# Optimization experiments

Hardware: AMD Instinct MI355X
Metric: run time of the kernel (lower is better)

Reference implementation:

```python
import jax, jax.numpy as jnp
import numpy as np

DIM, HEADS, HD, FFN = 1536, 12, 128, 8960
B, F, H, W = 1, 4, 20, 32
S = F * H * W          # 2560 latent tokens
L2 = 512               # text context length
EPS = 1e-6


def _ln(x):
    m = jnp.mean(x, -1, keepdims=True)
    v = jnp.mean(jnp.square(x - m), -1, keepdims=True)
    return (x - m) * jax.lax.rsqrt(v + EPS)


def _rms(x, g):
    return x * jax.lax.rsqrt(jnp.mean(jnp.square(x), -1, keepdims=True) + EPS) * g


def _dyn_quant(x):
    # per-token symmetric int8 dynamic activation quantization (A8, dynamic input scale)
    s = jnp.maximum(jnp.max(jnp.abs(x), -1, keepdims=True) / 127.0, 1e-8)
    q = jnp.clip(jnp.round(x / s), -127.0, 127.0)
    return q, s, jnp.sum(q, -1)   # sum_input used for asymmetric-weight zero-point correction


def _quant_w(w):
    # per-output-channel asymmetric int8 weight quantization (weight_sym=False)
    wmin = jnp.min(w, 1, keepdims=True)
    wmax = jnp.max(w, 1, keepdims=True)
    s = jnp.maximum((wmax - wmin) / 255.0, 1e-8)
    zp = jnp.round(-128.0 - wmin / s)
    qw = jnp.clip(jnp.round(w / s) + zp, -128.0, 127.0)
    return qw, s[:, 0], zp[:, 0]


def _w8a8(qx, s_x, sum_qx, w, b):
    # y = s_x * s_w * (qx @ (qw - zp)^T) + b = s_x*s_w*(qx@qw^T - zp*sum(qx)) + b
    qw, sw, zp = _quant_w(w)
    acc = jnp.einsum('bsi,oi->bso', qx, qw) - sum_qx[..., None] * zp
    return acc * s_x * sw + b


def _rope(x, fr, f, h, w):
    # x: [B,S,N,D] with S == f*h*w; fr: [1024, D//2] complex rope table
    Bn, Sn, N, D = x.shape
    c = D // 2
    s0 = c - 2 * (c // 3)
    fF = jnp.broadcast_to(fr[:f, :s0].reshape(f, 1, 1, s0), (f, h, w, s0))
    fH = jnp.broadcast_to(fr[:h, s0:s0 + c // 3].reshape(1, h, 1, c // 3), (f, h, w, c // 3))
    fW = jnp.broadcast_to(fr[:w, s0 + c // 3:].reshape(1, 1, w, c // 3), (f, h, w, c // 3))
    fi = jnp.concatenate([fF, fH, fW], -1).reshape(1, f * h * w, 1, c)
    xr = x.reshape(Bn, Sn, N, c, 2)
    xc = jax.lax.complex(xr[..., 0], xr[..., 1]) * fi
    return jnp.stack([jnp.real(xc), jnp.imag(xc)], -1).reshape(Bn, Sn, N, D)


def _attn(q, k, v, k_lens):
    scale = 1.0 / jnp.sqrt(jnp.float32(q.shape[-1]))
    scores = jnp.einsum('bqnd,bknd->bnqk', q, k) * scale
    mask = jnp.arange(k.shape[1])[None, None, None, :] < k_lens[:, None, None, None]
    p = jax.nn.softmax(jnp.where(mask, scores, -1e30), -1)
    return jnp.einsum('bnqk,bknd->bqnd', p, v)


def _forward(x, e, freqs, context, modulation,
             wq, bq, wk, bk, wv, bv, wo, bo, gq, gk, n3_w, n3_b,
             cwq, cbq, cwk, cbk, cwv, cbv, cwo, cbo, cgq, cgk,
             w1, b1, w2, b2, f, h, w, seq_lens, context_lens):
    fr = jax.lax.complex(freqs[..., 0], freqs[..., 1])
    em = modulation + e  # [B,6,C]
    sm, sc, gm, smlp, scmlp, gmlp = [em[:, i:i + 1] for i in range(6)]
    Bn, Sn, C = x.shape
    # --- self attention: fused norm+modulation then shared per-token int8 quant for q/k/v ---
    h1 = _ln(x) * (1.0 + sc) + sm
    qx, s_x, sum_qx = _dyn_quant(h1)
    q = _rms(_w8a8(qx, s_x, sum_qx, wq, bq), gq).reshape(Bn, Sn, HEADS, HD)
    k = _rms(_w8a8(qx, s_x, sum_qx, wk, bk), gk).reshape(Bn, Sn, HEADS, HD)
    v = _w8a8(qx, s_x, sum_qx, wv, bv).reshape(Bn, Sn, HEADS, HD)
    q = _rope(q, fr, f, h, w)
    k = _rope(k, fr, f, h, w)
    y = _attn(q, k, v, seq_lens).reshape(Bn, Sn, C) @ wo.T + bo
    x = x + y * gm
    # --- cross attention (fp16/fp path in the original; use_kernel[1]=False) ---
    hx = _ln(x) * n3_w + n3_b
    cq = _rms(hx @ cwq.T + cbq, cgq).reshape(Bn, Sn, HEADS, HD)
    ck = _rms(context @ cwk.T + cbk, cgk).reshape(Bn, L2, HEADS, HD)
    cv = (context @ cwv.T + cbv).reshape(Bn, L2, HEADS, HD)
    y = _attn(cq, ck, cv, context_lens).reshape(Bn, Sn, C) @ cwo.T + cbo
    x = x + y
    # --- FFN with modulation (use_kernel[2]=False) ---
    h2 = _ln(x) * (1.0 + scmlp) + smlp
    y = jax.nn.gelu(h2 @ w1.T + b1, approximate=True) @ w2.T + b2
    return x + y * gmlp


def setup_inputs():
    key = jax.random.key(0)
    ks = jax.random.split(key, 16)

    def P(i, shape, s=0.02):
        return jax.random.normal(ks[i], shape, jnp.float32) * s

    x = jax.random.normal(ks[0], (B, S, DIM), jnp.float32)
    e = jax.random.normal(ks[1], (B, 6, DIM), jnp.float32)
    context = jax.random.normal(ks[2], (B, L2, DIM), jnp.float32)
    seq_lens = jnp.array([S], jnp.int32)
    grid_sizes = jnp.array([[F, H, W]], jnp.int32)
    context_lens = jnp.array([L2], jnp.int32)
    c = HD // 2
    pos = np.arange(1024, dtype=np.float64)[:, None]
    theta = 1.0 / (10000.0 ** (np.arange(c, dtype=np.float64) / c))
    ang = pos * theta
    freqs = jnp.asarray(np.stack([np.cos(ang), np.sin(ang)], -1), jnp.float32)
    z = lambda n: jnp.zeros((n,), jnp.float32)
    o = lambda n: jnp.ones((n,), jnp.float32)
    return dict(x=x, e=e, seq_lens=seq_lens, grid_sizes=grid_sizes, freqs=freqs,
                context=context, context_lens=context_lens,
                modulation=P(3, (1, 6, DIM), 1.0 / DIM ** 0.5),
                wq=P(4, (DIM, DIM)), bq=z(DIM), wk=P(5, (DIM, DIM)), bk=z(DIM),
                wv=P(6, (DIM, DIM)), bv=z(DIM), wo=P(7, (DIM, DIM)), bo=z(DIM),
                gq=o(DIM), gk=o(DIM), n3_w=o(DIM), n3_b=z(DIM),
                cwq=P(8, (DIM, DIM)), cbq=z(DIM), cwk=P(9, (DIM, DIM)), cbk=z(DIM),
                cwv=P(10, (DIM, DIM)), cbv=z(DIM), cwo=P(11, (DIM, DIM)), cbo=z(DIM),
                cgq=o(DIM), cgk=o(DIM),
                w1=P(12, (FFN, DIM)), b1=z(FFN), w2=P(13, (DIM, FFN)), b2=z(DIM))


def reference(x, e, seq_lens, grid_sizes, freqs, context, context_lens, modulation,
              wq, bq, wk, bk, wv, bv, wo, bo, gq, gk, n3_w, n3_b,
              cwq, cbq, cwk, cbk, cwv, cbv, cwo, cbo, cgq, cgk,
              w1, b1, w2, b2):
    f, h, w = int(grid_sizes[0, 0]), int(grid_sizes[0, 1]), int(grid_sizes[0, 2])
    return _forward(x, e, freqs, context, modulation,
                    wq, bq, wk, bk, wv, bv, wo, bo, gq, gk, n3_w, n3_b,
                    cwq, cbq, cwk, cbk, cwv, cbv, cwo, cbo, cgq, cgk,
                    w1, b1, w2, b2, f, h, w, seq_lens, context_lens)
```

## Files before the change

### kernel.cpp

```cpp
#include <hip/hip_runtime.h>
#include <stdint.h>


typedef unsigned short u16;
typedef __bf16 bf16x8 __attribute__((ext_vector_type(8)));
typedef float f32x4 __attribute__((ext_vector_type(4)));

#define DEV __device__ __forceinline__

DEV u16 f2b(float f) {
  uint32_t u = __float_as_uint(f);
  u += 0x7fffu + ((u >> 16) & 1u);
  return (u16)(u >> 16);
}

DEV float gelu_tanh(float v) {
  float u = 0.7978845608028654f * (v + 0.044715f * v * v * v);
  return 0.5f * v * (1.0f + tanhf(u));
}

DEV void gl_lds16(const u16* g, u16* l) {
  __builtin_amdgcn_global_load_lds(
      (const __attribute__((address_space(1))) void*)g,
      (__attribute__((address_space(3))) void*)l, 16, 0, 0);
}

DEV float bred_sum(float v, float* scr) {
  #pragma unroll
  for (int o = 32; o; o >>= 1) v += __shfl_down(v, o, 64);
  if ((threadIdx.x & 63) == 0) scr[threadIdx.x >> 6] = v;
  __syncthreads();
  v = scr[0] + scr[1] + scr[2] + scr[3];
  __syncthreads();
  return v;
}
DEV float bred_max(float v, float* scr) {
  #pragma unroll
  for (int o = 32; o; o >>= 1) v = fmaxf(v, __shfl_down(v, o, 64));
  if ((threadIdx.x & 63) == 0) scr[threadIdx.x >> 6] = v;
  __syncthreads();
  v = fmaxf(fmaxf(scr[0], scr[1]), fmaxf(scr[2], scr[3]));
  __syncthreads();
  return v;
}
DEV float bred_min(float v, float* scr) {
  #pragma unroll
  for (int o = 32; o; o >>= 1) v = fminf(v, __shfl_down(v, o, 64));
  if ((threadIdx.x & 63) == 0) scr[threadIdx.x >> 6] = v;
  __syncthreads();
  v = fminf(fminf(scr[0], scr[1]), fminf(scr[2], scr[3]));
  __syncthreads();
  return v;
}

__global__ __launch_bounds__(256) void pack_kernel(
    const float* __restrict__ e, const float* __restrict__ mod,
    const float* __restrict__ cbk, const float* __restrict__ cbv,
    float* __restrict__ em, float* __restrict__ bckv) {
  int i = blockIdx.x * 256 + threadIdx.x;
  if (i < 9216) em[i] = e[i] + mod[i];
  if (i < 3072) bckv[i] = (i < 1536) ? cbk[i] : cbv[i - 1536];
}

__global__ __launch_bounds__(256) void cvt_bf16_kernel(
    const float* __restrict__ in, u16* __restrict__ out, int n4) {
  int stride = gridDim.x * 256;
  for (int i = blockIdx.x * 256 + threadIdx.x; i < n4; i += stride) {
    float4 v = ((const float4*)in)[i];
    uint2 r;
    r.x = (uint32_t)f2b(v.x) | ((uint32_t)f2b(v.y) << 16);
    r.y = (uint32_t)f2b(v.z) | ((uint32_t)f2b(v.w) << 16);
    ((uint2*)out)[i] = r;
  }
}

__global__ __launch_bounds__(256) void ln_quant_kernel(
    const float* __restrict__ x, const float* __restrict__ em,
    u16* __restrict__ qx, float* __restrict__ sx, float* __restrict__ sumq) {
  __shared__ float scr[4];
  const int row = blockIdx.x, tid = threadIdx.x;
  const float* xr = x + (size_t)row * 1536;
  float v[6], s = 0.f, s2 = 0.f;
  #pragma unroll
  for (int t = 0; t < 6; t++) { v[t] = xr[tid + t * 256]; s += v[t]; s2 += v[t] * v[t]; }
  s = bred_sum(s, scr); s2 = bred_sum(s2, scr);
  float mean = s / 1536.f;
  float var = s2 / 1536.f - mean * mean;
  float inv = rsqrtf(var + 1e-6f);
  float hv[6], amax = 0.f;
  #pragma unroll
  for (int t = 0; t < 6; t++) {
    int i = tid + t * 256;
    hv[t] = (v[t] - mean) * inv * (1.f + em[1536 + i]) + em[i];
    amax = fmaxf(amax, fabsf(hv[t]));
  }
  amax = bred_max(amax, scr);
  float sxv = fmaxf(amax / 127.f, 1e-8f);
  float qs = 0.f;
  #pragma unroll
  for (int t = 0; t < 6; t++) {
    int i = tid + t * 256;
    float q = fminf(fmaxf(rintf(hv[t] / sxv), -127.f), 127.f);
    qs += q;
    qx[(size_t)row * 1536 + i] = f2b(q);
  }
  qs = bred_sum(qs, scr);
  if (tid == 0) { sx[row] = sxv; sumq[row] = qs; }
}

__global__ __launch_bounds__(256) void quantw_kernel(
    const float* __restrict__ wq, const float* __restrict__ wk, const float* __restrict__ wv,
    const float* __restrict__ bq, const float* __restrict__ bk, const float* __restrict__ bv,
    u16* __restrict__ qw, float* __restrict__ sw, float* __restrict__ zp, float* __restrict__ ball) {
  __shared__ float scr[4];
  const int row = blockIdx.x, tid = threadIdx.x;
  const int sel = (row >= 3072) ? 2 : (row >= 1536 ? 1 : 0);
  const int r = row - sel * 1536;
  const float* w = sel == 0 ? wq : (sel == 1 ? wk : wv);
  const float* bb = sel == 0 ? bq : (sel == 1 ? bk : bv);
  const float* wr = w + (size_t)r * 1536;
  float v[6], mn = 1e30f, mx = -1e30f;
  #pragma unroll
  for (int t = 0; t < 6; t++) { v[t] = wr[tid + t * 256]; mn = fminf(mn, v[t]); mx = fmaxf(mx, v[t]); }
  mn = bred_min(mn, scr); mx = bred_max(mx, scr);
  float s = fmaxf((mx - mn) / 255.f, 1e-8f);
  float z = rintf(-128.f - mn / s);
  #pragma unroll
  for (int t = 0; t < 6; t++) {
    int i = tid + t * 256;
    float q = fminf(fmaxf(rintf(v[t] / s) + z, -128.f), 127.f);
    qw[(size_t)row * 1536 + i] = f2b(q);
  }
  if (tid == 0) { sw[row] = s; zp[row] = z; ball[row] = bb[r]; }
}

template<int EP>
DEV void gemm_epilogue(float v, int row, int col, int N, void* Cout,
                       const float* bias, const float* sxp, const float* sumqp,
                       const float* swp, const float* zpp,
                       const float* gp, const float* residp) {
  size_t idx = (size_t)row * N + col;
  if constexpr (EP == 0) {
    ((float*)Cout)[idx] = v + bias[col];
  } else if constexpr (EP == 1) {
    v = (v - sumqp[row] * zpp[col]) * (sxp[row] * swp[col]) + bias[col];
    ((float*)Cout)[idx] = v;
  } else if constexpr (EP == 2) {
    v += bias[col];
    if (gp) v *= gp[col];
    ((float*)Cout)[idx] = v + residp[idx];
  } else if constexpr (EP == 3) {
    ((u16*)Cout)[idx] = f2b(gelu_tanh(v + bias[col]));
  } else {
    ((float*)Cout)[idx] = v;
  }
}

template<int EP>
__global__ __launch_bounds__(256) void gemm_bt_kernel(
    const u16* __restrict__ A, const u16* __restrict__ B, void* __restrict__ Cout,
    int N, int K, const float* __restrict__ bias,
    const float* __restrict__ sxp, const float* __restrict__ sumqp,
    const float* __restrict__ swp, const float* __restrict__ zpp,
    const float* __restrict__ gp, const float* __restrict__ residp) {
  __shared__ __align__(16) u16 As[128 * 32];
  __shared__ __align__(16) u16 Bs[128 * 32];
  const int tid = threadIdx.x;
  const int wave = tid >> 6, lane = tid & 63;
  const int wm = wave >> 1, wn = wave & 1;
  const int quad = lane >> 4, l16 = lane & 15;
  const int m0 = blockIdx.y * 128, n0 = blockIdx.x * 128;

  int srow[2], scol[2];
  #pragma unroll
  for (int i = 0; i < 2; i++) {
    int row = (wave * 2 + i) * 16 + (lane >> 2);
    int chunk = ((lane & 3) - (row >> 1)) & 3;
    srow[i] = row; scol[i] = chunk * 8;
  }

  f32x4 acc[4][4];
  #pragma unroll
  for (int i = 0; i < 4; i++)
    #pragma unroll
    for (int j = 0; j < 4; j++) acc[i][j] = (f32x4){0.f, 0.f, 0.f, 0.f};

  for (int k0 = 0; k0 < K; k0 += 32) {
    #pragma unroll
    for (int i = 0; i < 2; i++) {
      gl_lds16(A + (size_t)(m0 + srow[i]) * K + k0 + scol[i], &As[(wave * 2 + i) * 512]);
      gl_lds16(B + (size_t)(n0 + srow[i]) * K + k0 + scol[i], &Bs[(wave * 2 + i) * 512]);
    }
    __syncthreads();
    bf16x8 af[4], bfv[4];
    #pragma unroll
    for (int mi = 0; mi < 4; mi++) {
      int row = wm * 64 + mi * 16 + l16;
      af[mi] = *(const bf16x8*)&As[row * 32 + (((quad + (row >> 1)) & 3) * 8)];
    }
    #pragma unroll
    for (int ni = 0; ni < 4; ni++) {
      int row = wn * 64 + ni * 16 + l16;
      bfv[ni] = *(const bf16x8*)&Bs[row * 32 + (((quad + (row >> 1)) & 3) * 8)];
    }
    #pragma unroll
    for (int mi = 0; mi < 4; mi++)
      #pragma unroll
      for (int ni = 0; ni < 4; ni++)
        acc[mi][ni] = __builtin_amdgcn_mfma_f32_16x16x32_bf16(af[mi], bfv[ni], acc[mi][ni], 0, 0, 0);
    __syncthreads();
  }
  #pragma unroll
  for (int mi = 0; mi < 4; mi++)
    #pragma unroll
    for (int ni = 0; ni < 4; ni++) {
      int col = n0 + wn * 64 + ni * 16 + l16;
      #pragma unroll
      for (int r = 0; r < 4; r++)
        gemm_epilogue<EP>(acc[mi][ni][r], m0 + wm * 64 + mi * 16 + quad * 4 + r, col,
                          N, Cout, bias, sxp, sumqp, swp, zpp, gp, residp);
    }
}

template<int EP>
__global__ __launch_bounds__(256) void gemm64_bt_kernel(
    const u16* __restrict__ A, const u16* __restrict__ B,
    void* __restrict__ Cout, void* __restrict__ Cout2, int N, int K, int KC,
    const float* __restrict__ bias,
    const float* __restrict__ sxp, const float* __restrict__ sumqp,
    const float* __restrict__ swp, const float* __restrict__ zpp,
    const float* __restrict__ gp, const float* __restrict__ residp) {
  __shared__ __align__(16) u16 As[2][64 * 64];
  __shared__ __align__(16) u16 Bs[2][128 * 64];
  const int tid = threadIdx.x;
  const int wave = tid >> 6, lane = tid & 63;
  const int wm = wave >> 1, wn = wave & 1;
  const int quad = lane >> 4, l16 = lane & 15;
  const int m0 = blockIdx.y * 64, n0 = blockIdx.x * 128;
  const int kstart = blockIdx.z * KC;

  int arow[2], acol[2], brow[4], bcol[4];
  #pragma unroll
  for (int i = 0; i < 2; i++) {
    int row = (wave * 2 + i) * 8 + (lane >> 3);
    arow[i] = row; acol[i] = (((lane & 7) - (row >> 1)) & 7) * 8;
  }
  #pragma unroll
  for (int i = 0; i < 4; i++) {
    int row = (wave * 4 + i) * 8 + (lane >> 3);
    brow[i] = row; bcol[i] = (((lane & 7) - (row >> 1)) & 7) * 8;
  }

  f32x4 acc[2][4];
  #pragma unroll
  for (int i = 0; i < 2; i++)
    #pragma unroll
    for (int j = 0; j < 4; j++) acc[i][j] = (f32x4){0.f, 0.f, 0.f, 0.f};

  const int nk = KC >> 6;
  auto stage = [&](int buf, int k0) {
    #pragma unroll
    for (int i = 0; i < 2; i++)
      gl_lds16(A + (size_t)(m0 + arow[i]) * K + kstart + k0 + acol[i],
               &As[buf][(wave * 2 + i) * 512]);
    #pragma unroll
    for (int i = 0; i < 4; i++)
      gl_lds16(B + (size_t)(n0 + brow[i]) * K + kstart + k0 + bcol[i],
               &Bs[buf][(wave * 4 + i) * 512]);
  };
  stage(0, 0);
  for (int kt = 0; kt < nk; kt++) {
    __syncthreads();
    const int cur = kt & 1;
    if (kt + 1 < nk) stage(1 - cur, (kt + 1) << 6);
    #pragma unroll
    for (int s = 0; s < 2; s++) {
      bf16x8 af[2], bfv[4];
      #pragma unroll
      for (int mi = 0; mi < 2; mi++) {
        int row = wm * 32 + mi * 16 + l16;
        int slot = ((s * 4 + quad) + (row >> 1)) & 7;
        af[mi] = *(const bf16x8*)&As[cur][row * 64 + slot * 8];
      }
      #pragma unroll
      for (int ni = 0; ni < 4; ni++) {
        int row = wn * 64 + ni * 16 + l16;
        int slot = ((s * 4 + quad) + (row >> 1)) & 7;
        bfv[ni] = *(const bf16x8*)&Bs[cur][row * 64 + slot * 8];
      }
      #pragma unroll
      for (int mi = 0; mi < 2; mi++)
        #pragma unroll
        for (int ni = 0; ni < 4; ni++)
          acc[mi][ni] = __builtin_amdgcn_mfma_f32_16x16x32_bf16(af[mi], bfv[ni], acc[mi][ni], 0, 0, 0);
    }
  }
  void* Cuse = (EP == 4 && blockIdx.z) ? Cout2 : Cout;
  #pragma unroll
  for (int mi = 0; mi < 2; mi++)
    #pragma unroll
    for (int ni = 0; ni < 4; ni++) {
      int col = n0 + wn * 64 + ni * 16 + l16;
      #pragma unroll
      for (int r = 0; r < 4; r++)
        gemm_epilogue<EP>(acc[mi][ni][r], m0 + wm * 32 + mi * 16 + quad * 4 + r, col,
                          N, Cuse, bias, sxp, sumqp, swp, zpp, gp, residp);
    }
}

__global__ __launch_bounds__(256) void splitk_reduce_kernel(
    const float* __restrict__ P0, const float* __restrict__ P1,
    float* __restrict__ out, const float* __restrict__ bias,
    const float* __restrict__ g, const float* __restrict__ resid,
    int N, int n4) {
  int stride = gridDim.x * 256;
  for (int i = blockIdx.x * 256 + threadIdx.x; i < n4; i += stride) {
    float4 a = ((const float4*)P0)[i];
    float4 b = ((const float4*)P1)[i];
    float4 r = ((const float4*)resid)[i];
    int col = (i * 4) % N;
    float4 o;
    o.x = (a.x + b.x + bias[col]) * g[col] + r.x;
    o.y = (a.y + b.y + bias[col + 1]) * g[col + 1] + r.y;
    o.z = (a.z + b.z + bias[col + 2]) * g[col + 2] + r.z;
    o.w = (a.w + b.w + bias[col + 3]) * g[col + 3] + r.w;
    ((float4*)out)[i] = o;
  }
}

__global__ __launch_bounds__(256) void rmsrope_b_kernel(
    const float* __restrict__ qkv, u16* __restrict__ qkvb,
    const float* __restrict__ gq, const float* __restrict__ gk,
    const float* __restrict__ freqs, const int* __restrict__ gsz) {
  __shared__ float scr[4];
  const int row = blockIdx.x, tid = threadIdx.x;
  const float* base = qkv + (size_t)row * 4608;
  u16* ob = qkvb + (size_t)row * 4608;
  const int gh = gsz[1], gw = gsz[2];
  const int hw = gh * gw;
  const int fi = row / hw, rem = row - fi * hw;
  const int hi = rem / gw, wi = rem - hi * gw;
  #pragma unroll
  for (int part = 0; part < 2; part++) {
    const float* p = base + part * 1536;
    u16* o = ob + part * 1536;
    const float* g = part ? gk : gq;
    const float sc = part ? 1.f : 0.08838834764831845f;
    float v[6], s2 = 0.f;
    #pragma unroll
    for (int t = 0; t < 6; t++) { v[t] = p[tid + t * 256]; s2 += v[t] * v[t]; }
    s2 = bred_sum(s2, scr);
    float inv = rsqrtf(s2 / 1536.f + 1e-6f);
    #pragma unroll
    for (int t = 0; t < 3; t++) {
      int pr = tid + t * 256;
      int c = pr & 63;
      int frow = (c < 22) ? fi : (c < 43 ? hi : wi);
      const float* fr = freqs + ((size_t)frow * 64 + c) * 2;
      float cv = fr[0], sv = fr[1];
      float x0 = p[2 * pr] * inv * g[2 * pr];
      float x1 = p[2 * pr + 1] * inv * g[2 * pr + 1];
      o[2 * pr] = f2b((x0 * cv - x1 * sv) * sc);
      o[2 * pr + 1] = f2b((x0 * sv + x1 * cv) * sc);
    }
  }
  #pragma unroll
  for (int t = 0; t < 6; t++) {
    int i = tid + t * 256;
    ob[3072 + i] = f2b(base[3072 + i]);
  }
}

__global__ __launch_bounds__(256) void rms_bf16_kernel(
    const float* __restrict__ X, u16* __restrict__ O, const float* __restrict__ g,
    int ldi, int ldo, float scale) {
  __shared__ float scr[4];
  const int row = blockIdx.x, tid = threadIdx.x;
  const float* xr = X + (size_t)row * ldi;
  u16* orow = O + (size_t)row * ldo;
  float v[6], s2 = 0.f;
  #pragma unroll
  for (int t = 0; t < 6; t++) { v[t] = xr[tid + t * 256]; s2 += v[t] * v[t]; }
  s2 = bred_sum(s2, scr);
  float inv = rsqrtf(s2 / 1536.f + 1e-6f) * scale;
  #pragma unroll
  for (int t = 0; t < 6; t++) {
    int i = tid + t * 256;
    orow[i] = f2b(v[t] * inv * g[i]);
  }
}

__global__ __launch_bounds__(256) void vtrans_kernel(
    const float* __restrict__ V, int ld, u16* __restrict__ Vt, int Skv) {
  __shared__ u16 T[64 * 136];
  const int h = blockIdx.y, k0 = blockIdx.x * 64, tid = threadIdx.x;
  #pragma unroll
  for (int i = 0; i < 8; i++) {
    int f4 = i * 256 + tid;
    int row = f4 >> 5, c4 = f4 & 31;
    float4 v = *(const float4*)(V + (size_t)(k0 + row) * ld + h * 128 + c4 * 4);
    ushort4 b;
    b.x = f2b(v.x); b.y = f2b(v.y); b.z = f2b(v.z); b.w = f2b(v.w);
    *(ushort4*)&T[row * 136 + c4 * 4] = b;
  }
  __syncthreads();
  #pragma unroll
  for (int i = 0; i < 4; i++) {
    int f8 = i * 256 + tid;
    int hd = f8 >> 3, kc = f8 & 7;
    u16 tmp[8];
    #pragma unroll
    for (int j = 0; j < 8; j++) tmp[j] = T[(kc * 8 + j) * 136 + hd];
    *(uint4*)(Vt + ((size_t)h * 128 + hd) * Skv + k0 + kc * 8) = *(const uint4*)tmp;
  }
}

__global__ __launch_bounds__(256) void fattn_kernel(
    const u16* __restrict__ Q, int ldq, const u16* __restrict__ Kg, int ldk,
    const u16* __restrict__ Vtg, u16* __restrict__ O, int ldo,
    const int* __restrict__ klen_ptr, int kmax) {
  __shared__ __align__(16) u16 Qs[64 * 136];
  __shared__ __align__(16) u16 Ks[64 * 136];
  __shared__ __align__(16) u16 Vt[128 * 72];
  __shared__ __align__(16) u16 Pt[4][16 * 72];
  const int tid = threadIdx.x, wave = tid >> 6, lane = tid & 63;
  const int quad = lane >> 4, l16 = lane & 15;
  const int h = blockIdx.y;
  const int q0 = blockIdx.x * 64;
  int klen = klen_ptr[0]; if (klen > kmax) klen = kmax;
  const u16* vbase = Vtg + (size_t)h * 128 * kmax;

  #pragma unroll
  for (int i = 0; i < 4; i++) {
    int c8 = i * 256 + tid;
    int row = c8 >> 4, cc = (c8 & 15) * 8;
    *(uint4*)&Qs[row * 136 + cc] = *(const uint4*)(Q + (size_t)(q0 + row) * ldq + h * 128 + cc);
  }
  __syncthreads();
  bf16x8 qf[4];
  #pragma unroll
  for (int s = 0; s < 4; s++)
    qf[s] = *(const bf16x8*)&Qs[(wave * 16 + l16) * 136 + s * 32 + quad * 8];

  float m_r[4] = {-1e30f, -1e30f, -1e30f, -1e30f};
  float l_r[4] = {0.f, 0.f, 0.f, 0.f};
  f32x4 oacc[8];
  #pragma unroll
  for (int n8 = 0; n8 < 8; n8++) oacc[n8] = (f32x4){0.f, 0.f, 0.f, 0.f};

  const int ktiles = (klen + 63) >> 6;
  for (int kt = 0; kt < ktiles; kt++) {
    const int k0 = kt * 64;
    __syncthreads();
    #pragma unroll
    for (int i = 0; i < 4; i++) {
      int c8 = i * 256 + tid;
      int row = c8 >> 4, cc = (c8 & 15) * 8;
      *(uint4*)&Ks[row * 136 + cc] = *(const uint4*)(Kg + (size_t)(k0 + row) * ldk + h * 128 + cc);
    }
    #pragma unroll
    for (int i = 0; i < 4; i++) {
      int f8 = i * 256 + tid;
      int hd = f8 >> 3, kc = f8 & 7;
      *(uint4*)&Vt[hd * 72 + kc * 8] = *(const uint4*)(vbase + (size_t)hd * kmax + k0 + kc * 8);
    }
    __syncthreads();
    f32x4 sacc[4];
    #pragma unroll
    for (int ni = 0; ni < 4; ni++) sacc[ni] = (f32x4){0.f, 0.f, 0.f, 0.f};
    #pragma unroll
    for (int ni = 0; ni < 4; ni++)
      #pragma unroll
      for (int s = 0; s < 4; s++) {
        bf16x8 kf = *(const bf16x8*)&Ks[(ni * 16 + l16) * 136 + s * 32 + quad * 8];
        sacc[ni] = __builtin_amdgcn_mfma_f32_16x16x32_bf16(qf[s], kf, sacc[ni], 0, 0, 0);
      }
    float alpha_r[4];
    #pragma unroll
    for (int r = 0; r < 4; r++) {
      float mx = -1e30f;
      #pragma unroll
      for (int ni = 0; ni < 4; ni++) {
        int col = k0 + ni * 16 + l16;
        float sv = (col < klen) ? sacc[ni][r] : -1e30f;
        sacc[ni][r] = sv;
        mx = fmaxf(mx, sv);
      }
      #pragma unroll
      for (int off = 1; off < 16; off <<= 1) mx = fmaxf(mx, __shfl_xor(mx, off, 64));
      float mnew = fmaxf(m_r[r], mx);
      float alpha = __expf(m_r[r] - mnew);
      float rsum = 0.f;
      float pv[4];
      #pragma unroll
      for (int ni = 0; ni < 4; ni++) {
        float p = __expf(sacc[ni][r] - mnew);
        pv[ni] = p;
        rsum += p;
      }
      #pragma unroll
      for (int off = 1; off < 16; off <<= 1) rsum += __shfl_xor(rsum, off, 64);
      l_r[r] = l_r[r] * alpha + rsum;
      m_r[r] = mnew;
      alpha_r[r] = alpha;
      #pragma unroll
      for (int ni = 0; ni < 4; ni++)
        Pt[wave][(quad * 4 + r) * 72 + ni * 16 + l16] = f2b(pv[ni]);
    }
    #pragma unroll
    for (int n8 = 0; n8 < 8; n8++)
      #pragma unroll
      for (int r = 0; r < 4; r++) oacc[n8][r] *= alpha_r[r];
    #pragma unroll
    for (int s2 = 0; s2 < 2; s2++) {
      bf16x8 pf = *(const bf16x8*)&Pt[wave][l16 * 72 + s2 * 32 + quad * 8];
      #pragma unroll
      for (int n8 = 0; n8 < 8; n8++) {
        bf16x8 vf = *(const bf16x8*)&Vt[(n8 * 16 + l16) * 72 + s2 * 32 + quad * 8];
        oacc[n8] = __builtin_amdgcn_mfma_f32_16x16x32_bf16(pf, vf, oacc[n8], 0, 0, 0);
      }
    }
  }
  float rl[4];
  #pragma unroll
  for (int r = 0; r < 4; r++) rl[r] = 1.f / l_r[r];
  #pragma unroll
  for (int n8 = 0; n8 < 8; n8++)
    #pragma unroll
    for (int r = 0; r < 4; r++) {
      int row = q0 + wave * 16 + quad * 4 + r;
      O[(size_t)row * ldo + h * 128 + n8 * 16 + l16] = f2b(oacc[n8][r] * rl[r]);
    }
}

__global__ __launch_bounds__(256) void ln_affine_kernel(
    const float* __restrict__ X, u16* __restrict__ O,
    const float* __restrict__ w, const float* __restrict__ b, float addone) {
  __shared__ float scr[4];
  const int row = blockIdx.x, tid = threadIdx.x;
  const float* xr = X + (size_t)row * 1536;
  float v[6], s = 0.f, s2 = 0.f;
  #pragma unroll
  for (int t = 0; t < 6; t++) { v[t] = xr[tid + t * 256]; s += v[t]; s2 += v[t] * v[t]; }
  s = bred_sum(s, scr); s2 = bred_sum(s2, scr);
  float mean = s / 1536.f;
  float inv = rsqrtf(s2 / 1536.f - mean * mean + 1e-6f);
  #pragma unroll
  for (int t = 0; t < 6; t++) {
    int i = tid + t * 256;
    O[(size_t)row * 1536 + i] = f2b((v[t] - mean) * inv * (addone + w[i]) + b[i]);
  }
}

extern "C" void kernel_launch(void* const* d_in, const int* in_sizes, int n_in,
                              void* d_out, int out_size, void* d_ws, size_t ws_size,
                              hipStream_t stream) {
  (void)in_sizes; (void)n_in; (void)out_size; (void)ws_size;
  const int S = 2560, D = 1536, L2C = 512, FF = 8960, ND = 4608, CKV = 3072;

  const float* x = (const float*)d_in[0];
  const float* e = (const float*)d_in[1];
  const int* seq_lens = (const int*)d_in[2];
  const int* grid_sz = (const int*)d_in[3];
  const float* freqs = (const float*)d_in[4];
  const float* context = (const float*)d_in[5];
  const int* ctx_lens = (const int*)d_in[6];
  const float* modulation = (const float*)d_in[7];
  const float* wq = (const float*)d_in[8];  const float* bq = (const float*)d_in[9];
  const float* wk = (const float*)d_in[10]; const float* bk = (const float*)d_in[11];
  const float* wv = (const float*)d_in[12]; const float* bv = (const float*)d_in[13];
  const float* wo = (const float*)d_in[14]; const float* bo = (const float*)d_in[15];
  const float* gq = (const float*)d_in[16]; const float* gk = (const float*)d_in[17];
  const float* n3w = (const float*)d_in[18]; const float* n3b = (const float*)d_in[19];
  const float* cwq = (const float*)d_in[20]; const float* cbq = (const float*)d_in[21];
  const float* cwk = (const float*)d_in[22]; const float* cbk = (const float*)d_in[23];
  const float* cwv = (const float*)d_in[24]; const float* cbv = (const float*)d_in[25];
  const float* cwo = (const float*)d_in[26]; const float* cbo = (const float*)d_in[27];
  const float* cgq = (const float*)d_in[28]; const float* cgk = (const float*)d_in[29];
  const float* w1 = (const float*)d_in[30]; const float* b1 = (const float*)d_in[31];
  const float* w2 = (const float*)d_in[32]; const float* b2 = (const float*)d_in[33];

  char* wsb = (char*)d_ws;
  size_t off = 0;
  auto alloc = [&](size_t bytes) -> void* {
    void* r = wsb + off;
    off += (bytes + 255) & ~(size_t)255;
    return r;
  };
  float* em   = (float*)alloc((size_t)6 * D * 4);
  float* bckv = (float*)alloc((size_t)CKV * 4);
  float* ball = (float*)alloc((size_t)ND * 4);
  float* sx   = (float*)alloc((size_t)S * 4);
  float* sumq = (float*)alloc((size_t)S * 4);
  float* sw   = (float*)alloc((size_t)ND * 4);
  float* zp   = (float*)alloc((size_t)ND * 4);
  u16* qx     = (u16*)alloc((size_t)S * D * 2);
  u16* qw     = (u16*)alloc((size_t)ND * D * 2);
  float* qkv  = (float*)alloc((size_t)S * ND * 4);
  u16* qkvb   = (u16*)alloc((size_t)S * ND * 2);
  u16* attnb  = (u16*)alloc((size_t)S * D * 2);
  u16* hx     = (u16*)alloc((size_t)S * D * 2);
  float* cq   = (float*)alloc((size_t)S * D * 4);
  float* ckv  = (float*)alloc((size_t)L2C * CKV * 4);
  u16* ctxb   = (u16*)alloc((size_t)L2C * D * 2);
  u16* cattn  = (u16*)alloc((size_t)S * D * 2);
  u16* wo_b   = (u16*)alloc((size_t)D * D * 2);
  u16* cwq_b  = (u16*)alloc((size_t)D * D * 2);
  u16* cwkv_b = (u16*)alloc((size_t)2 * D * D * 2);
  u16* cwo_b  = (u16*)alloc((size_t)D * D * 2);
  u16* w1_b   = (u16*)alloc((size_t)FF * D * 2);
  u16* w2_b   = (u16*)alloc((size_t)D * FF * 2);
  u16* h3 = (u16*)qkv;
  u16* h2 = attnb;
  u16* vtg = qw;
  u16* cvtg = qx;
  u16* cqb = hx;
  u16* ckvb = ctxb;
  float* x2 = cq;
  float* x1 = (float*)d_out;
  float* outp = (float*)d_out;
  float* P0 = (float*)qx;
  float* P1 = (float*)qkvb;

  auto cvt = [&](const float* in, u16* op, size_t n) {
    int n4 = (int)(n / 4);
    int blocks = (n4 + 255) / 256; if (blocks > 4096) blocks = 4096;
    cvt_bf16_kernel<<<blocks, 256, 0, stream>>>(in, op, n4);
  };

  pack_kernel<<<36, 256, 0, stream>>>(e, modulation, cbk, cbv, em, bckv);
  cvt(wo, wo_b, (size_t)D * D);
  cvt(cwq, cwq_b, (size_t)D * D);
  cvt(cwk, cwkv_b, (size_t)D * D);
  cvt(cwv, cwkv_b + (size_t)D * D, (size_t)D * D);
  cvt(cwo, cwo_b, (size_t)D * D);
  cvt(w1, w1_b, (size_t)FF * D);
  cvt(w2, w2_b, (size_t)D * FF);
  cvt(context, ctxb, (size_t)L2C * D);

  ln_quant_kernel<<<S, 256, 0, stream>>>(x, em, qx, sx, sumq);
  quantw_kernel<<<ND, 256, 0, stream>>>(wq, wk, wv, bq, bk, bv, qw, sw, zp, ball);

  gemm_bt_kernel<1><<<dim3(ND / 128, S / 128), 256, 0, stream>>>(
      qx, qw, qkv, ND, D, ball, sx, sumq, sw, zp, nullptr, nullptr);

  rmsrope_b_kernel<<<S, 256, 0, stream>>>(qkv, qkvb, gq, gk, freqs, grid_sz);
  vtrans_kernel<<<dim3(S / 64, 12), 256, 0, stream>>>(qkv + 3072, ND, vtg, S);

  fattn_kernel<<<dim3(S / 64, 12), 256, 0, stream>>>(
      qkvb, ND, qkvb + 1536, ND, vtg, attnb, D, seq_lens, S);

  gemm64_bt_kernel<2><<<dim3(D / 128, S / 64), 256, 0, stream>>>(
      attnb, wo_b, x1, nullptr, D, D, D, bo, nullptr, nullptr, nullptr, nullptr, em + 2 * D, x);

  ln_affine_kernel<<<S, 256, 0, stream>>>(x1, hx, n3w, n3b, 0.f);

  gemm64_bt_kernel<0><<<dim3(D / 128, S / 64), 256, 0, stream>>>(
      hx, cwq_b, cq, nullptr, D, D, D, cbq, nullptr, nullptr, nullptr, nullptr, nullptr, nullptr);
  gemm64_bt_kernel<0><<<dim3(CKV / 128, L2C / 64), 256, 0, stream>>>(
      ctxb, cwkv_b, ckv, nullptr, CKV, D, D, bckv, nullptr, nullptr, nullptr, nullptr, nullptr, nullptr);

  rms_bf16_kernel<<<S, 256, 0, stream>>>(cq, cqb, cgq, D, D, 0.08838834764831845f);
  rms_bf16_kernel<<<L2C, 256, 0, stream>>>(ckv, ckvb, cgk, CKV, D, 1.f);
  vtrans_kernel<<<dim3(L2C / 64, 12), 256, 0, stream>>>(ckv + 1536, CKV, cvtg, L2C);

  fattn_kernel<<<dim3(S / 64, 12), 256, 0, stream>>>(
      cqb, D, ckvb, D, cvtg, cattn, D, ctx_lens, L2C);

  gemm64_bt_kernel<2><<<dim3(D / 128, S / 64), 256, 0, stream>>>(
      cattn, cwo_b, x2, nullptr, D, D, D, cbo, nullptr, nullptr, nullptr, nullptr, nullptr, x1);

  ln_affine_kernel<<<S, 256, 0, stream>>>(x2, h2, em + 4 * D, em + 3 * D, 1.f);

  gemm_bt_kernel<3><<<dim3(FF / 128, S / 128), 256, 0, stream>>>(
      h2, w1_b, h3, FF, D, b1, nullptr, nullptr, nullptr, nullptr, nullptr, nullptr);

  gemm64_bt_kernel<4><<<dim3(D / 128, S / 64, 2), 256, 0, stream>>>(
      h3, w2_b, P0, P1, D, FF, FF / 2, nullptr, nullptr, nullptr, nullptr, nullptr, nullptr, nullptr);
  splitk_reduce_kernel<<<960, 256, 0, stream>>>(
      P0, P1, outp, b2, em + 5 * D, x2, D, S * D / 4);
}
```

Baseline: 941.5 us.

## Replace 128-tile GEMMs with 256x256 double-buffered 8-wave GEMM, split-K by four

```diff
diff --git a/kernel.cpp b/kernel.cpp
--- a/kernel.cpp
+++ b/kernel.cpp
@@ -156,69 +156,137 @@
   }
 }
 
+struct PtrQuad { void* p0; void* p1; void* p2; void* p3; };
+
 template<int EP>
-__global__ __launch_bounds__(256) void gemm_bt_kernel(
-    const u16* __restrict__ A, const u16* __restrict__ B, void* __restrict__ Cout,
-    int N, int K, const float* __restrict__ bias,
+__global__ __launch_bounds__(512, 2) void gemm256_bt_kernel(
+    const u16* __restrict__ A, const u16* __restrict__ B, PtrQuad pq,
+    int N, int K, int KC,
+    const float* __restrict__ bias,
     const float* __restrict__ sxp, const float* __restrict__ sumqp,
-    const float* __restrict__ swp, const float* __restrict__ zpp,
-    const float* __restrict__ gp, const float* __restrict__ residp) {
-  __shared__ __align__(16) u16 As[128 * 32];
-  __shared__ __align__(16) u16 Bs[128 * 32];
+    const float* __restrict__ swp, const float* __restrict__ zpp) {
+  __shared__ __align__(16) u16 As[2][256 * 64];
+  __shared__ __align__(16) u16 Bs[2][256 * 64];
   const int tid = threadIdx.x;
   const int wave = tid >> 6, lane = tid & 63;
-  const int wm = wave >> 1, wn = wave & 1;
+  const int wm = wave >> 2, wn = wave & 3;
   const int quad = lane >> 4, l16 = lane & 15;
-  const int m0 = blockIdx.y * 128, n0 = blockIdx.x * 128;
-
-  int srow[2], scol[2];
-  #pragma unroll
-  for (int i = 0; i < 2; i++) {
-    int row = (wave * 2 + i) * 16 + (lane >> 2);
-    int chunk = ((lane & 3) - (row >> 1)) & 3;
-    srow[i] = row; scol[i] = chunk * 8;
-  }
-
-  f32x4 acc[4][4];
-  #pragma unroll
-  for (int i = 0; i < 4; i++)
+
+  const int gx = gridDim.x, gy = gridDim.y;
+  const int nwg = gx * gy * (int)gridDim.z;
+  const int orig = ((int)blockIdx.z * gy + (int)blockIdx.y) * gx + (int)blockIdx.x;
+  const int qq = nwg >> 3, rr = nwg & 7, xcd = orig & 7, lin = orig >> 3;
+  const int wg = (xcd < rr ? xcd * (qq + 1) : rr * (qq + 1) + (xcd - rr) * qq) + lin;
+  const int bx = wg % gx, t2 = wg / gx, by = t2 % gy, bz = t2 / gy;
+  const int m0 = by * 256, n0 = bx * 256;
+
+  const u16* Abase = A + (size_t)m0 * K + (size_t)bz * KC;
+  const u16* Bbase = B + (size_t)n0 * K + (size_t)bz * KC;
+
+  const u16* ap[4]; const u16* bp[4];
+  #pragma unroll
+  for (int i = 0; i < 4; i++) {
+    int idx = i * 512 + tid;
+    int row = idx >> 3;
+    int col = ((idx & 7) ^ (row & 7)) * 8;
+    ap[i] = Abase + (size_t)row * K + col;
+    bp[i] = Bbase + (size_t)row * K + col;
+  }
+
+  f32x4 acc[8][4];
+  #pragma unroll
+  for (int i = 0; i < 8; i++)
     #pragma unroll
     for (int j = 0; j < 4; j++) acc[i][j] = (f32x4){0.f, 0.f, 0.f, 0.f};
 
-  for (int k0 = 0; k0 < K; k0 += 32) {
-    #pragma unroll
-    for (int i = 0; i < 2; i++) {
-      gl_lds16(A + (size_t)(m0 + srow[i]) * K + k0 + scol[i], &As[(wave * 2 + i) * 512]);
-      gl_lds16(B + (size_t)(n0 + srow[i]) * K + k0 + scol[i], &Bs[(wave * 2 + i) * 512]);
-    }
-    __syncthreads();
-    bf16x8 af[4], bfv[4];
-    #pragma unroll
-    for (int mi = 0; mi < 4; mi++) {
-      int row = wm * 64 + mi * 16 + l16;
-      af[mi] = *(const bf16x8*)&As[row * 32 + (((quad + (row >> 1)) & 3) * 8)];
-    }
-    #pragma unroll
-    for (int ni = 0; ni < 4; ni++) {
-      int row = wn * 64 + ni * 16 + l16;
-      bfv[ni] = *(const bf16x8*)&Bs[row * 32 + (((quad + (row >> 1)) & 3) * 8)];
-    }
-    #pragma unroll
-    for (int mi = 0; mi < 4; mi++)
-      #pragma unroll
-      for (int ni = 0; ni < 4; ni++)
-        acc[mi][ni] = __builtin_amdgcn_mfma_f32_16x16x32_bf16(af[mi], bfv[ni], acc[mi][ni], 0, 0, 0);
-    __syncthreads();
-  }
-  #pragma unroll
-  for (int mi = 0; mi < 4; mi++)
+  auto stA = [&](int buf, int kt) {
+    #pragma unroll
+    for (int i = 0; i < 4; i++)
+      gl_lds16(ap[i] + (kt << 6), &As[buf][(i * 512 + wave * 64) * 8]);
+  };
+  auto stB = [&](int buf, int kt) {
+    #pragma unroll
+    for (int i = 0; i < 4; i++)
+      gl_lds16(bp[i] + (kt << 6), &Bs[buf][(i * 512 + wave * 64) * 8]);
+  };
+
+  bf16x8 afr[4][2], bfr[2][2];
+  auto ldA = [&](int cur, int mh) {
+    #pragma unroll
+    for (int f = 0; f < 4; f++) {
+      int row = wm * 128 + mh * 64 + f * 16 + l16;
+      int rx = row & 7;
+      #pragma unroll
+      for (int kk = 0; kk < 2; kk++)
+        afr[f][kk] = *(const bf16x8*)&As[cur][row * 64 + (((kk * 4 + quad) ^ rx) << 3)];
+    }
+  };
+  auto ldB = [&](int cur, int nh) {
+    #pragma unroll
+    for (int f = 0; f < 2; f++) {
+      int row = wn * 64 + nh * 32 + f * 16 + l16;
+      int rx = row & 7;
+      #pragma unroll
+      for (int kk = 0; kk < 2; kk++)
+        bfr[f][kk] = *(const bf16x8*)&Bs[cur][row * 64 + (((kk * 4 + quad) ^ rx) << 3)];
+    }
+  };
+  auto mmaQ = [&](int mh, int nh) {
+    __builtin_amdgcn_s_setprio(1);
+    #pragma unroll
+    for (int kk = 0; kk < 2; kk++)
+      #pragma unroll
+      for (int f = 0; f < 4; f++)
+        #pragma unroll
+        for (int g = 0; g < 2; g++)
+          acc[mh * 4 + f][nh * 2 + g] = __builtin_amdgcn_mfma_f32_16x16x32_bf16(
+              afr[f][kk], bfr[g][kk], acc[mh * 4 + f][nh * 2 + g], 0, 0, 0);
+    __builtin_amdgcn_s_setprio(0);
+  };
+
+  const int nk = KC >> 6;
+  stA(0, 0); stB(0, 0);
+  asm volatile("s_waitcnt vmcnt(0)" ::: "memory");
+  __builtin_amdgcn_s_barrier();
+
+  for (int kt = 0; kt < nk; kt++) {
+    const int cur = kt & 1, nxt = cur ^ 1;
+    const bool pf = (kt + 1 < nk);
+    ldA(cur, 0); ldB(cur, 0);
+    if (pf) stA(nxt, kt + 1);
+    __builtin_amdgcn_s_barrier();
+    mmaQ(0, 0);
+    __builtin_amdgcn_s_barrier();
+    ldB(cur, 1);
+    if (pf) stB(nxt, kt + 1);
+    __builtin_amdgcn_s_barrier();
+    mmaQ(0, 1);
+    __builtin_amdgcn_s_barrier();
+    ldA(cur, 1);
+    __builtin_amdgcn_s_barrier();
+    mmaQ(1, 1);
+    __builtin_amdgcn_s_barrier();
+    ldB(cur, 0);
+    __builtin_amdgcn_s_barrier();
+    mmaQ(1, 0);
+    if (pf) asm volatile("s_waitcnt vmcnt(0)" ::: "memory");
+    __builtin_amdgcn_s_barrier();
+  }
+
+  void* Cuse;
+  if constexpr (EP == 4)
+    Cuse = bz == 0 ? pq.p0 : (bz == 1 ? pq.p1 : (bz == 2 ? pq.p2 : pq.p3));
+  else
+    Cuse = pq.p0;
+  #pragma unroll
+  for (int mi = 0; mi < 8; mi++)
     #pragma unroll
     for (int ni = 0; ni < 4; ni++) {
       int col = n0 + wn * 64 + ni * 16 + l16;
       #pragma unroll
       for (int r = 0; r < 4; r++)
-        gemm_epilogue<EP>(acc[mi][ni][r], m0 + wm * 64 + mi * 16 + quad * 4 + r, col,
-                          N, Cout, bias, sxp, sumqp, swp, zpp, gp, residp);
+        gemm_epilogue<EP>(acc[mi][ni][r], m0 + wm * 128 + mi * 16 + quad * 4 + r, col,
+                          N, Cuse, bias, sxp, sumqp, swp, zpp, nullptr, nullptr);
     }
 }
 
@@ -308,8 +376,9 @@
     }
 }
 
-__global__ __launch_bounds__(256) void splitk_reduce_kernel(
+__global__ __launch_bounds__(256) void splitk_reduce4_kernel(
     const float* __restrict__ P0, const float* __restrict__ P1,
+    const float* __restrict__ P2, const float* __restrict__ P3,
     float* __restrict__ out, const float* __restrict__ bias,
     const float* __restrict__ g, const float* __restrict__ resid,
     int N, int n4) {
@@ -317,13 +386,15 @@
   for (int i = blockIdx.x * 256 + threadIdx.x; i < n4; i += stride) {
     float4 a = ((const float4*)P0)[i];
     float4 b = ((const float4*)P1)[i];
+    float4 c = ((const float4*)P2)[i];
+    float4 d = ((const float4*)P3)[i];
     float4 r = ((const float4*)resid)[i];
     int col = (i * 4) % N;
     float4 o;
-    o.x = (a.x + b.x + bias[col]) * g[col] + r.x;
-    o.y = (a.y + b.y + bias[col + 1]) * g[col + 1] + r.y;
-    o.z = (a.z + b.z + bias[col + 2]) * g[col + 2] + r.z;
-    o.w = (a.w + b.w + bias[col + 3]) * g[col + 3] + r.w;
+    o.x = (a.x + b.x + c.x + d.x + bias[col]) * g[col] + r.x;
+    o.y = (a.y + b.y + c.y + d.y + bias[col + 1]) * g[col + 1] + r.y;
+    o.z = (a.z + b.z + c.z + d.z + bias[col + 2]) * g[col + 2] + r.z;
+    o.w = (a.w + b.w + c.w + d.w + bias[col + 3]) * g[col + 3] + r.w;
     ((float4*)out)[i] = o;
   }
 }
@@ -621,6 +692,8 @@
   float* outp = (float*)d_out;
   float* P0 = (float*)qx;
   float* P1 = (float*)qkvb;
+  float* P2 = (float*)attnb;
+  float* P3 = (float*)cattn;
 
   auto cvt = [&](const float* in, u16* op, size_t n) {
     int n4 = (int)(n / 4);
@@ -641,8 +714,11 @@
   ln_quant_kernel<<<S, 256, 0, stream>>>(x, em, qx, sx, sumq);
   quantw_kernel<<<ND, 256, 0, stream>>>(wq, wk, wv, bq, bk, bv, qw, sw, zp, ball);
 
-  gemm_bt_kernel<1><<<dim3(ND / 128, S / 128), 256, 0, stream>>>(
-      qx, qw, qkv, ND, D, ball, sx, sumq, sw, zp, nullptr, nullptr);
+  {
+    PtrQuad pq{qkv, nullptr, nullptr, nullptr};
+    gemm256_bt_kernel<1><<<dim3(ND / 256, S / 256), 512, 0, stream>>>(
+        qx, qw, pq, ND, D, D, ball, sx, sumq, sw, zp);
+  }
 
   rmsrope_b_kernel<<<S, 256, 0, stream>>>(qkv, qkvb, gq, gk, freqs, grid_sz);
   vtrans_kernel<<<dim3(S / 64, 12), 256, 0, stream>>>(qkv + 3072, ND, vtg, S);
@@ -672,11 +748,17 @@
 
   ln_affine_kernel<<<S, 256, 0, stream>>>(x2, h2, em + 4 * D, em + 3 * D, 1.f);
 
-  gemm_bt_kernel<3><<<dim3(FF / 128, S / 128), 256, 0, stream>>>(
-      h2, w1_b, h3, FF, D, b1, nullptr, nullptr, nullptr, nullptr, nullptr, nullptr);
-
-  gemm64_bt_kernel<4><<<dim3(D / 128, S / 64, 2), 256, 0, stream>>>(
-      h3, w2_b, P0, P1, D, FF, FF / 2, nullptr, nullptr, nullptr, nullptr, nullptr, nullptr, nullptr);
-  splitk_reduce_kernel<<<960, 256, 0, stream>>>(
-      P0, P1, outp, b2, em + 5 * D, x2, D, S * D / 4);
-}
+  {
+    PtrQuad pq{h3, nullptr, nullptr, nullptr};
+    gemm256_bt_kernel<3><<<dim3(FF / 256, S / 256), 512, 0, stream>>>(
+        h2, w1_b, pq, FF, D, D, b1, nullptr, nullptr, nullptr, nullptr);
+  }
+
+  {
+    PtrQuad pq{P0, P1, P2, P3};
+    gemm256_bt_kernel<4><<<dim3(D / 256, S / 256, 4), 512, 0, stream>>>(
+        h3, w2_b, pq, D, FF, FF / 4, nullptr, nullptr, nullptr, nullptr, nullptr);
+  }
+  splitk_reduce4_kernel<<<960, 256, 0, stream>>>(
+      P0, P1, P2, P3, outp, b2, em + 5 * D, x2, D, S * D / 4);
+}
```

New measurement: 908.5 us. 3.5% less time.
